# Performance work log

Measured on AMD Instinct MI355X. Metric: run time of the kernel, lower is better.

Reference implementation:

```python
import jax, jax.numpy as jnp
import numpy as np

B, Q, K = 4, 1024, 2048
QDIM, MDIM, EDIM, H = 1024, 1024, 1024, 16
HD = EDIM // H

def setup_inputs() -> dict:
    key = jax.random.key(0)
    ks = jax.random.split(key, 7)
    s = lambda d: (1.0 / np.sqrt(d))
    return {
        'query': jax.random.normal(ks[0], (B, Q, QDIM), jnp.float32),
        'memory': jax.random.normal(ks[1], (B, K, MDIM), jnp.float32),
        'bias': jax.random.normal(ks[2], (B, K), jnp.float32),
        'Wq': jax.random.normal(ks[3], (QDIM, EDIM), jnp.float32) * s(QDIM),
        'Wk': jax.random.normal(ks[4], (MDIM, EDIM), jnp.float32) * s(MDIM),
        'Wv': jax.random.normal(ks[5], (MDIM, EDIM), jnp.float32) * s(MDIM),
        'Wo': jax.random.normal(ks[6], (EDIM, EDIM), jnp.float32) * s(EDIM),
    }

def reference(query, memory, bias, Wq, Wk, Wv, Wo):
    scale = HD ** -0.5
    # projections -> [B, H, Q/K, HD]
    q = (query @ Wq).reshape(B, Q, H, HD).transpose(0, 2, 1, 3)
    k = (memory @ Wk).reshape(B, K, H, HD).transpose(0, 2, 1, 3)
    v = (memory @ Wv).reshape(B, K, H, HD).transpose(0, 2, 1, 3)
    scores = jnp.einsum('bhqd,bhkd->bhqk', q, k) * scale
    scores = scores + bias[:, None, None, :]
    weights = jax.nn.softmax(scores, axis=-1)
    out = jnp.einsum('bhqk,bhkd->bhqd', weights, v)
    out = out.transpose(0, 2, 1, 3).reshape(B, Q, EDIM)
    return out @ Wo
```

## Files before the change

kernel.cpp:

```cpp
#include <hip/hip_runtime.h>
#include <cstdint>
#include <cstddef>

typedef unsigned short u16;
typedef __attribute__((ext_vector_type(8))) short bf16x8;
typedef __attribute__((ext_vector_type(4))) short bf16x4;
typedef __attribute__((ext_vector_type(4))) float f32x4;
typedef __attribute__((ext_vector_type(16))) float f32x16;

#define B_  4
#define Q_  1024
#define K_  2048
#define E_  1024
#define H_  16
#define HD_ 64
#define LOG2E 1.4426950408889634f
#define M0_  16.0f

__device__ inline u16 f2bf(float f) {
  union { float f; uint32_t u; } x; x.f = f;
  return (u16)((x.u + 0x7fffu + ((x.u >> 16) & 1u)) >> 16);
}

__device__ inline short bfc(float f) {
  __bf16 h = (__bf16)f;
  return __builtin_bit_cast(short, h);
}

__device__ inline void gload16(const u16* g, void* l) {
  __builtin_amdgcn_global_load_lds((const __attribute__((address_space(1))) void*)g,
                                   (__attribute__((address_space(3))) void*)l, 16, 0, 0);
}

#define NQ8 (B_ * Q_ * E_ / 8)
#define NM8 (B_ * K_ * E_ / 8)
#define NBI (B_ * K_)
#define NPREP ((NQ8 + NM8 + NBI) / 256)
__global__ __launch_bounds__(256) void prep_all(const float* __restrict__ query,
                                                const float* __restrict__ memory,
                                                const float* __restrict__ bias,
                                                const float* W0, const float* W1,
                                                const float* W2, const float* W3,
                                                u16* __restrict__ qb,
                                                u16* __restrict__ mb,
                                                float* __restrict__ bias2,
                                                u16* T0, u16* T1, u16* T2, u16* T3) {
  __shared__ float t[64][65];
  int bid = blockIdx.x;
  if (bid < NPREP) {
    int i = bid * 256 + threadIdx.x;
    const float* src;
    u16* dst;
    if (i < NQ8) {
      src = query + (size_t)i * 8; dst = qb + (size_t)i * 8;
    } else if (i < NQ8 + NM8) {
      int j = i - NQ8;
      src = memory + (size_t)j * 8; dst = mb + (size_t)j * 8;
    } else {
      int j = i - (NQ8 + NM8);
      if (j < NBI) bias2[j] = bias[j] * LOG2E - M0_;
      return;
    }
    float4 a = *reinterpret_cast<const float4*>(src);
    float4 b = *reinterpret_cast<const float4*>(src + 4);
    union { u16 u[8]; uint4 v; } r;
    r.u[0] = f2bf(a.x); r.u[1] = f2bf(a.y); r.u[2] = f2bf(a.z); r.u[3] = f2bf(a.w);
    r.u[4] = f2bf(b.x); r.u[5] = f2bf(b.y); r.u[6] = f2bf(b.z); r.u[7] = f2bf(b.w);
    *reinterpret_cast<uint4*>(dst) = r.v;
  } else {
    int tb = bid - NPREP;
    int z = tb >> 8, xy = tb & 255;
    const float* W; u16* T;
    switch (z) {
      case 0: W = W0; T = T0; break;
      case 1: W = W1; T = T1; break;
      case 2: W = W2; T = T2; break;
      default: W = W3; T = T3; break;
    }
    int k0 = (xy & 15) * 64, n0 = (xy >> 4) * 64;
    int r = threadIdx.x >> 6, c = threadIdx.x & 63;
#pragma unroll
    for (int i = 0; i < 16; ++i)
      t[r + i * 4][c] = W[(size_t)(k0 + r + i * 4) * E_ + n0 + c];
    __syncthreads();
#pragma unroll
    for (int i = 0; i < 16; ++i)
      T[(size_t)(n0 + r + i * 4) * E_ + k0 + c] = f2bf(t[c][r + i * 4]);
  }
}

template <int MODE>
__device__ __forceinline__ void gemm_body(const u16* __restrict__ A,
                                          const u16* __restrict__ Bt,
                                          void* __restrict__ C,
                                          int M, int N, int Kc, int bx, int by,
                                          char* lds) {
  const int tid = threadIdx.x;
  const int w = tid >> 6, l = tid & 63;
  const int wr = w >> 1, wc = w & 1;
  const int lr = l & 15, lg = l >> 4;
  const int m0 = bx * 128, n0 = by * 128;

  const int e0g = tid * 8, e1g = e0g + 2048;
  const int row0 = e0g >> 5, row1 = e1g >> 5;
  const int lc0 = ((((e0g & 31) >> 3) ^ ((row0 >> 1) & 3)) * 8);
  const int lc1 = ((((e1g & 31) >> 3) ^ ((row1 >> 1) & 3)) * 8);
  const u16* Ar0 = A  + (size_t)(m0 + row0) * Kc + lc0;
  const u16* Ar1 = A  + (size_t)(m0 + row1) * Kc + lc1;
  const u16* Br0 = Bt + (size_t)(n0 + row0) * Kc + lc0;
  const u16* Br1 = Bt + (size_t)(n0 + row1) * Kc + lc1;
  const int d0 = tid * 16, d1 = d0 + 4096;

  const int ck = (lg ^ ((lr >> 1) & 3)) * 16;
  const int aofs = (wr * 64 + lr) * 64 + ck;
  const int bofs = (wc * 64 + lr) * 64 + ck;

  f32x4 acc[4][4];
#pragma unroll
  for (int mt = 0; mt < 4; ++mt)
#pragma unroll
    for (int nt = 0; nt < 4; ++nt)
      acc[mt][nt] = (f32x4){0.f, 0.f, 0.f, 0.f};

  gload16(Ar0, lds + d0);
  gload16(Ar1, lds + d1);
  gload16(Br0, lds + 24576 + d0);
  gload16(Br1, lds + 24576 + d1);
  gload16(Ar0 + 32, lds + 8192 + d0);
  gload16(Ar1 + 32, lds + 8192 + d1);
  gload16(Br0 + 32, lds + 24576 + 8192 + d0);
  gload16(Br1 + 32, lds + 24576 + 8192 + d1);
  asm volatile("s_waitcnt vmcnt(4)" ::: "memory");
  __builtin_amdgcn_s_barrier();

  const int NI = Kc >> 5;
  int rb = 0, wb = 16384;
  for (int ki = 0; ki < NI; ++ki) {
    if (ki + 2 < NI) {
      const int kk = (ki + 2) * 32;
      gload16(Ar0 + kk, lds + wb + d0);
      gload16(Ar1 + kk, lds + wb + d1);
      gload16(Br0 + kk, lds + 24576 + wb + d0);
      gload16(Br1 + kk, lds + 24576 + wb + d1);
    }

    bf16x8 a[4], b[4];
#pragma unroll
    for (int mt = 0; mt < 4; ++mt)
      a[mt] = *reinterpret_cast<const bf16x8*>(lds + rb + aofs + mt * 1024);
#pragma unroll
    for (int nt = 0; nt < 4; ++nt)
      b[nt] = *reinterpret_cast<const bf16x8*>(lds + 24576 + rb + bofs + nt * 1024);
    __builtin_amdgcn_s_setprio(1);
#pragma unroll
    for (int mt = 0; mt < 4; ++mt)
#pragma unroll
      for (int nt = 0; nt < 4; ++nt)
        acc[mt][nt] = __builtin_amdgcn_mfma_f32_16x16x32_bf16(a[mt], b[nt], acc[mt][nt], 0, 0, 0);
    __builtin_amdgcn_s_setprio(0);

    if (ki + 2 < NI) {
      asm volatile("s_waitcnt vmcnt(4)" ::: "memory");
    } else {
      asm volatile("s_waitcnt vmcnt(0)" ::: "memory");
    }
    __builtin_amdgcn_s_barrier();
    rb = (rb == 16384) ? 0 : rb + 8192;
    wb = (wb == 16384) ? 0 : wb + 8192;
  }

#pragma unroll
  for (int mt = 0; mt < 4; ++mt) {
#pragma unroll
    for (int nt = 0; nt < 4; ++nt) {
      int col = n0 + wc * 64 + nt * 16 + lr;
#pragma unroll
      for (int j = 0; j < 4; ++j) {
        int row = m0 + wr * 64 + mt * 16 + lg * 4 + j;
        float v = acc[mt][nt][j];
        if (MODE == 1) {
          ((u16*)C)[(size_t)row * N + col] = f2bf(v);
        } else if (MODE == 3) {
          ((u16*)C)[(size_t)row * N + col] = f2bf(v * (0.125f * LOG2E));
        } else {
          ((u16*)C)[((size_t)((col >> 11) * 16 + (row >> 6)) * 64 + (row & 63)) * 2048 + (col & 2047)] = f2bf(v);
        }
      }
    }
  }
}

__global__ __launch_bounds__(512) void gemm_out(const u16* __restrict__ A,
                                                const u16* __restrict__ Bt,
                                                float* __restrict__ C,
                                                int N, int Kc) {
  __shared__ uint4 lds4[3072];
  char* lds = (char*)lds4;
  int d = blockIdx.x;
  int bid = (d & 7) * 32 + (d >> 3);
  const int bx = bid >> 3, by = bid & 7;
  const int tid = threadIdx.x;
  const int w = tid >> 6, l = tid & 63;
  const int wrow = w >> 2, wcol = w & 3;
  const int lr = l & 15, lg = l >> 4;
  const int m0 = bx * 128, n0 = by * 128;

  const int e = tid * 8;
  const int row = e >> 5;
  const int lc = ((((e & 31) >> 3) ^ ((row >> 1) & 3)) * 8);
  const u16* Ar = A  + (size_t)(m0 + row) * Kc + lc;
  const u16* Br = Bt + (size_t)(n0 + row) * Kc + lc;
  const int dd = tid * 16;

  const int ck = (lg ^ ((lr >> 1) & 3)) * 16;
  const int aofs = (wrow * 64 + lr) * 64 + ck;
  const int bofs = (wcol * 32 + lr) * 64 + ck;

  f32x4 acc[4][2];
#pragma unroll
  for (int mt = 0; mt < 4; ++mt)
#pragma unroll
    for (int nt = 0; nt < 2; ++nt)
      acc[mt][nt] = (f32x4){0.f, 0.f, 0.f, 0.f};

  gload16(Ar, lds + dd);
  gload16(Br, lds + 24576 + dd);
  gload16(Ar + 32, lds + 8192 + dd);
  gload16(Br + 32, lds + 24576 + 8192 + dd);
  asm volatile("s_waitcnt vmcnt(2)" ::: "memory");
  __builtin_amdgcn_s_barrier();

  const int NI = Kc >> 5;
  int rb = 0, wb = 16384;
  for (int ki = 0; ki < NI; ++ki) {
    if (ki + 2 < NI) {
      const int kk = (ki + 2) * 32;
      gload16(Ar + kk, lds + wb + dd);
      gload16(Br + kk, lds + 24576 + wb + dd);
    }

    bf16x8 a[4], b[2];
#pragma unroll
    for (int mt = 0; mt < 4; ++mt)
      a[mt] = *reinterpret_cast<const bf16x8*>(lds + rb + aofs + mt * 1024);
#pragma unroll
    for (int nt = 0; nt < 2; ++nt)
      b[nt] = *reinterpret_cast<const bf16x8*>(lds + 24576 + rb + bofs + nt * 1024);
    __builtin_amdgcn_s_setprio(1);
#pragma unroll
    for (int mt = 0; mt < 4; ++mt)
#pragma unroll
      for (int nt = 0; nt < 2; ++nt)
        acc[mt][nt] = __builtin_amdgcn_mfma_f32_16x16x32_bf16(a[mt], b[nt], acc[mt][nt], 0, 0, 0);
    __builtin_amdgcn_s_setprio(0);

    if (ki + 2 < NI) {
      asm volatile("s_waitcnt vmcnt(2)" ::: "memory");
    } else {
      asm volatile("s_waitcnt vmcnt(0)" ::: "memory");
    }
    __builtin_amdgcn_s_barrier();
    rb = (rb == 16384) ? 0 : rb + 8192;
    wb = (wb == 16384) ? 0 : wb + 8192;
  }

#pragma unroll
  for (int mt = 0; mt < 4; ++mt) {
#pragma unroll
    for (int nt = 0; nt < 2; ++nt) {
      int col = n0 + wcol * 32 + nt * 16 + lr;
#pragma unroll
      for (int j = 0; j < 4; ++j) {
        int rowc = m0 + wrow * 64 + mt * 16 + lg * 4 + j;
        C[(size_t)rowc * N + col] = acc[mt][nt][j];
      }
    }
  }
}

__global__ __launch_bounds__(256) void proj_fused(const u16* __restrict__ qb,
                                                  const u16* __restrict__ mb,
                                                  const u16* __restrict__ wqt,
                                                  const u16* __restrict__ wkt,
                                                  const u16* __restrict__ wvt,
                                                  u16* __restrict__ qproj,
                                                  u16* __restrict__ kproj,
                                                  u16* __restrict__ vt) {
  __shared__ uint4 lds4[3072];
  char* lds = (char*)lds4;
  int d = blockIdx.x;
  int bid = (d & 7) * 160 + (d >> 3);
  if (bid < 256) {
    gemm_body<3>(qb, wqt, qproj, B_ * Q_, E_, E_, bid >> 3, bid & 7, lds);
  } else if (bid < 768) {
    int i = bid - 256;
    gemm_body<1>(mb, wkt, kproj, B_ * K_, E_, E_, i >> 3, i & 7, lds);
  } else {
    int i = bid - 768;
    gemm_body<2>(wvt, mb, vt, E_, B_ * K_, E_, i & 7, i >> 3, lds);
  }
}

__global__ __launch_bounds__(256, 4) void attn_kernel(const u16* __restrict__ qp,
                                                      const u16* __restrict__ kp,
                                                      const u16* __restrict__ vT,
                                                      const float* __restrict__ bias2,
                                                      u16* __restrict__ out) {
  __shared__ uint4 lds4[2048];
  char* ldsb = (char*)lds4;

  const int blk = blockIdx.x;
  const int hg = blk & 63, qt = blk >> 6;
  const int b = hg >> 4, h = hg & 15;
  const int tid = threadIdx.x;
  const int w = tid >> 6, l = tid & 63;
  const int wq = w & 1, wk = w >> 1;
  const int l31 = l & 31, lh = l >> 5;

  const int bk4 = l31 >> 2;
  const int t4 = bk4 & 3;
  const int pk31 = (((t4 == 1) || (t4 == 2)) ? (bk4 ^ 3) : bk4) * 4 + (l31 & 3);

  bf16x8 qf[4];
  const u16* qrow = qp + (size_t)(b * Q_ + qt * 64 + wq * 32 + l31) * E_ + h * 64 + lh * 8;
#pragma unroll
  for (int st = 0; st < 4; ++st)
    qf[st] = *reinterpret_cast<const bf16x8*>(qrow + st * 16);

  f32x16 O0, O1;
#pragma unroll
  for (int i = 0; i < 16; ++i) { O0[i] = 0.f; O1[i] = 0.f; }
  float OsumL = 0.f;

  const float* bias_b = bias2 + (size_t)b * K_;
  const u16* kbase = kp + (size_t)b * K_ * E_ + h * 64;
  const u16* vbase = vT + (size_t)(b * H_ + h) * HD_ * K_;

  const int xkk = (pk31 & 7) * 8;
  const int xvv = (l31 & 7) * 8;
  int kofs[4];
#pragma unroll
  for (int st = 0; st < 4; ++st)
    kofs[st] = (wk * 32 + pk31) * 128 + (((st * 16 + lh * 8) ^ xkk) << 1);
  int vofs[2];
#pragma unroll
  for (int ksl = 0; ksl < 2; ++ksl)
    vofs[ksl] = 16384 + l31 * 128 + (((wk * 32 + ksl * 16 + lh * 8) ^ xvv) << 1);

  const float* btp = bias_b + wk * 32 + lh * 8;
  float4 bg0 = *reinterpret_cast<const float4*>(btp);
  float4 bg1 = *reinterpret_cast<const float4*>(btp + 4);
  float4 bg2 = *reinterpret_cast<const float4*>(btp + 16);
  float4 bg3 = *reinterpret_cast<const float4*>(btp + 20);

  const int e0 = tid * 8, e1 = e0 + 2048;
  const int r0 = e0 >> 6, r1 = e1 >> 6;
  const int sc0 = (e0 & 63) ^ ((r0 & 7) * 8);
  const int sc1 = (e1 & 63) ^ ((r1 & 7) * 8);
  const u16* kp0 = kbase + (size_t)r0 * E_ + sc0;
  const u16* kp1 = kbase + (size_t)r1 * E_ + sc1;
  const u16* vp0 = vbase + (size_t)r0 * K_ + sc0;
  const u16* vp1 = vbase + (size_t)r1 * K_ + sc1;

  gload16(kp0, ldsb + tid * 16);
  gload16(kp1, ldsb + 4096 + tid * 16);
  gload16(vp0, ldsb + 16384 + tid * 16);
  gload16(vp1, ldsb + 16384 + 4096 + tid * 16);
  __syncthreads();

  const int NT = K_ / 64;
  for (int t = 0; t < NT; ++t) {
    if (t + 1 < NT) {
      const int nb = ((t & 1) ^ 1) * 8192;
      kp0 += (size_t)64 * E_; kp1 += (size_t)64 * E_;
      vp0 += 64; vp1 += 64;
      gload16(kp0, ldsb + nb + tid * 16);
      gload16(kp1, ldsb + nb + 4096 + tid * 16);
      gload16(vp0, ldsb + 16384 + nb + tid * 16);
      gload16(vp1, ldsb + 16384 + nb + 4096 + tid * 16);
    }

    f32x16 S;
    S[0] = bg0.x; S[1] = bg0.y; S[2] = bg0.z; S[3] = bg0.w;
    S[4] = bg1.x; S[5] = bg1.y; S[6] = bg1.z; S[7] = bg1.w;
    S[8] = bg2.x; S[9] = bg2.y; S[10] = bg2.z; S[11] = bg2.w;
    S[12] = bg3.x; S[13] = bg3.y; S[14] = bg3.z; S[15] = bg3.w;

    float4 ng0 = bg0, ng1 = bg1, ng2 = bg2, ng3 = bg3;
    if (t + 1 < NT) {
      btp += 64;
      ng0 = *reinterpret_cast<const float4*>(btp);
      ng1 = *reinterpret_cast<const float4*>(btp + 4);
      ng2 = *reinterpret_cast<const float4*>(btp + 16);
      ng3 = *reinterpret_cast<const float4*>(btp + 20);
    }

    __builtin_amdgcn_s_setprio(1);
#pragma unroll
    for (int st = 0; st < 4; ++st) {
      bf16x8 ka = *reinterpret_cast<const bf16x8*>(ldsb + kofs[st]);
      S = __builtin_amdgcn_mfma_f32_32x32x16_bf16(ka, qf[st], S, 0, 0, 0);
    }
    __builtin_amdgcn_s_setprio(0);

#pragma unroll
    for (int i = 0; i < 16; ++i) S[i] = __builtin_amdgcn_exp2f(S[i]);
    float ps = ((S[0] + S[1]) + (S[2] + S[3])) + ((S[4] + S[5]) + (S[6] + S[7]))
             + ((S[8] + S[9]) + (S[10] + S[11])) + ((S[12] + S[13]) + (S[14] + S[15]));
    OsumL += ps;

    uint32_t u[8];
#pragma unroll
    for (int j = 0; j < 8; ++j) {
      float plo = S[2 * j], phi = S[2 * j + 1];
      asm("v_cvt_pk_bf16_f32 %0, %1, %2" : "=v"(u[j]) : "v"(plo), "v"(phi));
    }
    bf16x8 P0 = __builtin_bit_cast(bf16x8, (uint4){u[0], u[1], u[2], u[3]});
    bf16x8 P1 = __builtin_bit_cast(bf16x8, (uint4){u[4], u[5], u[6], u[7]});

    __builtin_amdgcn_s_setprio(1);
    {
      bf16x8 va;
      va = *reinterpret_cast<const bf16x8*>(ldsb + vofs[0]);
      O0 = __builtin_amdgcn_mfma_f32_32x32x16_bf16(va, P0, O0, 0, 0, 0);
      va = *reinterpret_cast<const bf16x8*>(ldsb + vofs[0] + 4096);
      O1 = __builtin_amdgcn_mfma_f32_32x32x16_bf16(va, P0, O1, 0, 0, 0);
      va = *reinterpret_cast<const bf16x8*>(ldsb + vofs[1]);
      O0 = __builtin_amdgcn_mfma_f32_32x32x16_bf16(va, P1, O0, 0, 0, 0);
      va = *reinterpret_cast<const bf16x8*>(ldsb + vofs[1] + 4096);
      O1 = __builtin_amdgcn_mfma_f32_32x32x16_bf16(va, P1, O1, 0, 0, 0);
    }
    __builtin_amdgcn_s_setprio(0);

    bg0 = ng0; bg1 = ng1; bg2 = ng2; bg3 = ng3;
    kofs[0] ^= 8192; kofs[1] ^= 8192; kofs[2] ^= 8192; kofs[3] ^= 8192;
    vofs[0] ^= 8192; vofs[1] ^= 8192;
    __syncthreads();
  }

  float Osum = OsumL + __shfl_xor(OsumL, 32, 64);

  float* ex = (float*)ldsb + (size_t)(wq * 64 + l) * 33;
  if (wk == 1) {
#pragma unroll
    for (int i = 0; i < 16; ++i) ex[i] = O0[i];
#pragma unroll
    for (int i = 0; i < 16; ++i) ex[16 + i] = O1[i];
    ex[32] = Osum;
  }
  __syncthreads();
  if (wk == 0) {
#pragma unroll
    for (int i = 0; i < 16; ++i) O0[i] += ex[i];
#pragma unroll
    for (int i = 0; i < 16; ++i) O1[i] += ex[16 + i];
    Osum += ex[32];
    float inv = 1.f / Osum;
    u16* orow = out + (size_t)(b * Q_ + qt * 64 + wq * 32 + l31) * E_ + h * 64;
#pragma unroll
    for (int g = 0; g < 4; ++g) {
      int hd0 = 8 * g + 4 * lh;
#pragma unroll
      for (int j = 0; j < 4; ++j) {
        orow[hd0 + j] = (u16)bfc(O0[4 * g + j] * inv);
        orow[32 + hd0 + j] = (u16)bfc(O1[4 * g + j] * inv);
      }
    }
  }
}

extern "C" void kernel_launch(void* const* d_in, const int* in_sizes, int n_in,
                              void* d_out, int out_size, void* d_ws, size_t ws_size,
                              hipStream_t stream) {
  const float* query  = (const float*)d_in[0];
  const float* memory = (const float*)d_in[1];
  const float* bias   = (const float*)d_in[2];
  const float* Wq     = (const float*)d_in[3];
  const float* Wk     = (const float*)d_in[4];
  const float* Wv     = (const float*)d_in[5];
  const float* Wo     = (const float*)d_in[6];
  float* out = (float*)d_out;

  char* p = (char*)d_ws;
  u16* qb    = (u16*)p; p += (size_t)B_ * Q_ * E_ * 2;
  u16* mb    = (u16*)p; p += (size_t)B_ * K_ * E_ * 2;
  u16* wqt   = (u16*)p; p += (size_t)E_ * E_ * 2;
  u16* wkt   = (u16*)p; p += (size_t)E_ * E_ * 2;
  u16* wvt   = (u16*)p; p += (size_t)E_ * E_ * 2;
  u16* wot   = (u16*)p; p += (size_t)E_ * E_ * 2;
  u16* qproj = (u16*)p; p += (size_t)B_ * Q_ * E_ * 2;
  u16* kproj = (u16*)p; p += (size_t)B_ * K_ * E_ * 2;
  u16* vt    = (u16*)p; p += (size_t)B_ * K_ * E_ * 2;
  u16* attn  = (u16*)p; p += (size_t)B_ * Q_ * E_ * 2;
  float* bias2 = (float*)p; p += (size_t)B_ * K_ * 4;

  prep_all<<<NPREP + 1024, 256, 0, stream>>>(query, memory, bias, Wq, Wk, Wv, Wo,
                                             qb, mb, bias2, wqt, wkt, wvt, wot);

  proj_fused<<<1280, 256, 0, stream>>>(qb, mb, wqt, wkt, wvt, qproj, kproj, vt);

  attn_kernel<<<B_ * H_ * (Q_ / 64), 256, 0, stream>>>(qproj, kproj, vt, bias2, attn);

  gemm_out<<<256, 512, 0, stream>>>(attn, wot, out, E_, E_);
}
```

Baseline: 134.9 us.

## Fuse fp32-to-bf16 conversion of activations into projection GEMM loads

Removes the separate pass that converted query and memory to bf16 buffers. The projection GEMM now reads fp32 directly, converts in registers and stores to LDS, which saves a full write and re-read of the activations. The LDS pipeline also drops from triple buffering with async global-to-LDS loads to double buffering with register staging and a __syncthreads every iteration. That may expose more latency, and the memory operand is now read as fp32 by both the K and V GEMMs.

```diff
diff --git a/kernel.cpp b/kernel.cpp
--- a/kernel.cpp
+++ b/kernel.cpp
@@ -16,6 +16,7 @@
 #define HD_ 64
 #define LOG2E 1.4426950408889634f
 #define M0_  16.0f
+#define NBI (B_ * K_)
 
 __device__ inline u16 f2bf(float f) {
   union { float f; uint32_t u; } x; x.f = f;
@@ -27,73 +28,52 @@
   return __builtin_bit_cast(short, h);
 }
 
+__device__ inline uint2 pack4(float4 a) {
+  union { u16 u[4]; uint2 v; } r;
+  r.u[0] = (u16)bfc(a.x); r.u[1] = (u16)bfc(a.y);
+  r.u[2] = (u16)bfc(a.z); r.u[3] = (u16)bfc(a.w);
+  return r.v;
+}
+
 __device__ inline void gload16(const u16* g, void* l) {
   __builtin_amdgcn_global_load_lds((const __attribute__((address_space(1))) void*)g,
                                    (__attribute__((address_space(3))) void*)l, 16, 0, 0);
 }
 
-#define NQ8 (B_ * Q_ * E_ / 8)
-#define NM8 (B_ * K_ * E_ / 8)
-#define NBI (B_ * K_)
-#define NPREP ((NQ8 + NM8 + NBI) / 256)
-__global__ __launch_bounds__(256) void prep_all(const float* __restrict__ query,
-                                                const float* __restrict__ memory,
-                                                const float* __restrict__ bias,
+__global__ __launch_bounds__(256) void prep_all(const float* __restrict__ bias,
                                                 const float* W0, const float* W1,
                                                 const float* W2, const float* W3,
-                                                u16* __restrict__ qb,
-                                                u16* __restrict__ mb,
                                                 float* __restrict__ bias2,
                                                 u16* T0, u16* T1, u16* T2, u16* T3) {
   __shared__ float t[64][65];
   int bid = blockIdx.x;
-  if (bid < NPREP) {
-    int i = bid * 256 + threadIdx.x;
-    const float* src;
-    u16* dst;
-    if (i < NQ8) {
-      src = query + (size_t)i * 8; dst = qb + (size_t)i * 8;
-    } else if (i < NQ8 + NM8) {
-      int j = i - NQ8;
-      src = memory + (size_t)j * 8; dst = mb + (size_t)j * 8;
-    } else {
-      int j = i - (NQ8 + NM8);
-      if (j < NBI) bias2[j] = bias[j] * LOG2E - M0_;
-      return;
-    }
-    float4 a = *reinterpret_cast<const float4*>(src);
-    float4 b = *reinterpret_cast<const float4*>(src + 4);
-    union { u16 u[8]; uint4 v; } r;
-    r.u[0] = f2bf(a.x); r.u[1] = f2bf(a.y); r.u[2] = f2bf(a.z); r.u[3] = f2bf(a.w);
-    r.u[4] = f2bf(b.x); r.u[5] = f2bf(b.y); r.u[6] = f2bf(b.z); r.u[7] = f2bf(b.w);
-    *reinterpret_cast<uint4*>(dst) = r.v;
-  } else {
-    int tb = bid - NPREP;
-    int z = tb >> 8, xy = tb & 255;
-    const float* W; u16* T;
-    switch (z) {
-      case 0: W = W0; T = T0; break;
-      case 1: W = W1; T = T1; break;
-      case 2: W = W2; T = T2; break;
-      default: W = W3; T = T3; break;
-    }
-    int k0 = (xy & 15) * 64, n0 = (xy >> 4) * 64;
-    int r = threadIdx.x >> 6, c = threadIdx.x & 63;
-#pragma unroll
-    for (int i = 0; i < 16; ++i)
-      t[r + i * 4][c] = W[(size_t)(k0 + r + i * 4) * E_ + n0 + c];
-    __syncthreads();
-#pragma unroll
-    for (int i = 0; i < 16; ++i)
-      T[(size_t)(n0 + r + i * 4) * E_ + k0 + c] = f2bf(t[c][r + i * 4]);
-  }
-}
-
-template <int MODE>
-__device__ __forceinline__ void gemm_body(const u16* __restrict__ A,
-                                          const u16* __restrict__ Bt,
-                                          void* __restrict__ C,
-                                          int M, int N, int Kc, int bx, int by,
+  if (bid >= 1024) {
+    int j = (bid - 1024) * 256 + threadIdx.x;
+    if (j < NBI) bias2[j] = bias[j] * LOG2E - M0_;
+    return;
+  }
+  int z = bid >> 8, xy = bid & 255;
+  const float* W; u16* T;
+  switch (z) {
+    case 0: W = W0; T = T0; break;
+    case 1: W = W1; T = T1; break;
+    case 2: W = W2; T = T2; break;
+    default: W = W3; T = T3; break;
+  }
+  int k0 = (xy & 15) * 64, n0 = (xy >> 4) * 64;
+  int r = threadIdx.x >> 6, c = threadIdx.x & 63;
+#pragma unroll
+  for (int i = 0; i < 16; ++i)
+    t[r + i * 4][c] = W[(size_t)(k0 + r + i * 4) * E_ + n0 + c];
+  __syncthreads();
+#pragma unroll
+  for (int i = 0; i < 16; ++i)
+    T[(size_t)(n0 + r + i * 4) * E_ + k0 + c] = f2bf(t[c][r + i * 4]);
+}
+
+template <int MODE, bool AF32, bool BF32>
+__device__ __forceinline__ void gemm_body(const void* Ap, const void* Bp,
+                                          void* C, int M, int N, int Kc, int bx, int by,
                                           char* lds) {
   const int tid = threadIdx.x;
   const int w = tid >> 6, l = tid & 63;
@@ -105,15 +85,31 @@
   const int row0 = e0g >> 5, row1 = e1g >> 5;
   const int lc0 = ((((e0g & 31) >> 3) ^ ((row0 >> 1) & 3)) * 8);
   const int lc1 = ((((e1g & 31) >> 3) ^ ((row1 >> 1) & 3)) * 8);
-  const u16* Ar0 = A  + (size_t)(m0 + row0) * Kc + lc0;
-  const u16* Ar1 = A  + (size_t)(m0 + row1) * Kc + lc1;
-  const u16* Br0 = Bt + (size_t)(n0 + row0) * Kc + lc0;
-  const u16* Br1 = Bt + (size_t)(n0 + row1) * Kc + lc1;
   const int d0 = tid * 16, d1 = d0 + 4096;
 
+  const int fr = tid >> 3;
+  const int fcb = (tid & 7) * 4;
+  const int fphys = ((fcb >> 3) ^ ((fr >> 1) & 3));
+  const int fdst = fr * 64 + fphys * 16 + (fcb & 7) * 2;
+
+  const u16* A16_0 = nullptr; const u16* A16_1 = nullptr; const float* Afp = nullptr;
+  const u16* B16_0 = nullptr; const u16* B16_1 = nullptr; const float* Bfp = nullptr;
+  if constexpr (AF32) {
+    Afp = (const float*)Ap + (size_t)(m0 + fr) * Kc + fcb;
+  } else {
+    A16_0 = (const u16*)Ap + (size_t)(m0 + row0) * Kc + lc0;
+    A16_1 = (const u16*)Ap + (size_t)(m0 + row1) * Kc + lc1;
+  }
+  if constexpr (BF32) {
+    Bfp = (const float*)Bp + (size_t)(n0 + fr) * Kc + fcb;
+  } else {
+    B16_0 = (const u16*)Bp + (size_t)(n0 + row0) * Kc + lc0;
+    B16_1 = (const u16*)Bp + (size_t)(n0 + row1) * Kc + lc1;
+  }
+
   const int ck = (lg ^ ((lr >> 1) & 3)) * 16;
-  const int aofs = (wr * 64 + lr) * 64 + ck;
-  const int bofs = (wc * 64 + lr) * 64 + ck;
+  int aofs = (wr * 64 + lr) * 64 + ck;
+  int bofs = 16384 + (wc * 64 + lr) * 64 + ck;
 
   f32x4 acc[4][4];
 #pragma unroll
@@ -122,35 +118,71 @@
     for (int nt = 0; nt < 4; ++nt)
       acc[mt][nt] = (f32x4){0.f, 0.f, 0.f, 0.f};
 
-  gload16(Ar0, lds + d0);
-  gload16(Ar1, lds + d1);
-  gload16(Br0, lds + 24576 + d0);
-  gload16(Br1, lds + 24576 + d1);
-  gload16(Ar0 + 32, lds + 8192 + d0);
-  gload16(Ar1 + 32, lds + 8192 + d1);
-  gload16(Br0 + 32, lds + 24576 + 8192 + d0);
-  gload16(Br1 + 32, lds + 24576 + 8192 + d1);
-  asm volatile("s_waitcnt vmcnt(4)" ::: "memory");
-  __builtin_amdgcn_s_barrier();
+  if constexpr (AF32) {
+    float4 t0 = *reinterpret_cast<const float4*>(Afp);
+    float4 t1 = *reinterpret_cast<const float4*>(Afp + (size_t)32 * Kc);
+    float4 t2 = *reinterpret_cast<const float4*>(Afp + (size_t)64 * Kc);
+    float4 t3 = *reinterpret_cast<const float4*>(Afp + (size_t)96 * Kc);
+    *reinterpret_cast<uint2*>(lds + fdst)        = pack4(t0);
+    *reinterpret_cast<uint2*>(lds + fdst + 2048) = pack4(t1);
+    *reinterpret_cast<uint2*>(lds + fdst + 4096) = pack4(t2);
+    *reinterpret_cast<uint2*>(lds + fdst + 6144) = pack4(t3);
+  } else {
+    gload16(A16_0, lds + d0);
+    gload16(A16_1, lds + d1);
+  }
+  if constexpr (BF32) {
+    float4 t0 = *reinterpret_cast<const float4*>(Bfp);
+    float4 t1 = *reinterpret_cast<const float4*>(Bfp + (size_t)32 * Kc);
+    float4 t2 = *reinterpret_cast<const float4*>(Bfp + (size_t)64 * Kc);
+    float4 t3 = *reinterpret_cast<const float4*>(Bfp + (size_t)96 * Kc);
+    *reinterpret_cast<uint2*>(lds + 16384 + fdst)        = pack4(t0);
+    *reinterpret_cast<uint2*>(lds + 16384 + fdst + 2048) = pack4(t1);
+    *reinterpret_cast<uint2*>(lds + 16384 + fdst + 4096) = pack4(t2);
+    *reinterpret_cast<uint2*>(lds + 16384 + fdst + 6144) = pack4(t3);
+  } else {
+    gload16(B16_0, lds + 16384 + d0);
+    gload16(B16_1, lds + 16384 + d1);
+  }
+  __syncthreads();
 
   const int NI = Kc >> 5;
-  int rb = 0, wb = 16384;
+  int cur = 0;
   for (int ki = 0; ki < NI; ++ki) {
-    if (ki + 2 < NI) {
-      const int kk = (ki + 2) * 32;
-      gload16(Ar0 + kk, lds + wb + d0);
-      gload16(Ar1 + kk, lds + wb + d1);
-      gload16(Br0 + kk, lds + 24576 + wb + d0);
-      gload16(Br1 + kk, lds + 24576 + wb + d1);
+    const int nb = (cur ^ 1) * 8192;
+    const bool pf = (ki + 1 < NI);
+    float4 va0, va1, va2, va3, vb0, vb1, vb2, vb3;
+    if (pf) {
+      const int kk = (ki + 1) * 32;
+      if constexpr (AF32) {
+        const float* s = Afp + kk;
+        va0 = *reinterpret_cast<const float4*>(s);
+        va1 = *reinterpret_cast<const float4*>(s + (size_t)32 * Kc);
+        va2 = *reinterpret_cast<const float4*>(s + (size_t)64 * Kc);
+        va3 = *reinterpret_cast<const float4*>(s + (size_t)96 * Kc);
+      } else {
+        gload16(A16_0 + kk, lds + nb + d0);
+        gload16(A16_1 + kk, lds + nb + d1);
+      }
+      if constexpr (BF32) {
+        const float* s = Bfp + kk;
+        vb0 = *reinterpret_cast<const float4*>(s);
+        vb1 = *reinterpret_cast<const float4*>(s + (size_t)32 * Kc);
+        vb2 = *reinterpret_cast<const float4*>(s + (size_t)64 * Kc);
+        vb3 = *reinterpret_cast<const float4*>(s + (size_t)96 * Kc);
+      } else {
+        gload16(B16_0 + kk, lds + 16384 + nb + d0);
+        gload16(B16_1 + kk, lds + 16384 + nb + d1);
+      }
     }
 
     bf16x8 a[4], b[4];
 #pragma unroll
     for (int mt = 0; mt < 4; ++mt)
-      a[mt] = *reinterpret_cast<const bf16x8*>(lds + rb + aofs + mt * 1024);
+      a[mt] = *reinterpret_cast<const bf16x8*>(lds + aofs + mt * 1024);
 #pragma unroll
     for (int nt = 0; nt < 4; ++nt)
-      b[nt] = *reinterpret_cast<const bf16x8*>(lds + 24576 + rb + bofs + nt * 1024);
+      b[nt] = *reinterpret_cast<const bf16x8*>(lds + bofs + nt * 1024);
     __builtin_amdgcn_s_setprio(1);
 #pragma unroll
     for (int mt = 0; mt < 4; ++mt)
@@ -159,14 +191,23 @@
         acc[mt][nt] = __builtin_amdgcn_mfma_f32_16x16x32_bf16(a[mt], b[nt], acc[mt][nt], 0, 0, 0);
     __builtin_amdgcn_s_setprio(0);
 
-    if (ki + 2 < NI) {
-      asm volatile("s_waitcnt vmcnt(4)" ::: "memory");
-    } else {
-      asm volatile("s_waitcnt vmcnt(0)" ::: "memory");
-    }
-    __builtin_amdgcn_s_barrier();
-    rb = (rb == 16384) ? 0 : rb + 8192;
-    wb = (wb == 16384) ? 0 : wb + 8192;
+    if (pf) {
+      if constexpr (AF32) {
+        *reinterpret_cast<uint2*>(lds + nb + fdst)        = pack4(va0);
+        *reinterpret_cast<uint2*>(lds + nb + fdst + 2048) = pack4(va1);
+        *reinterpret_cast<uint2*>(lds + nb + fdst + 4096) = pack4(va2);
+        *reinterpret_cast<uint2*>(lds + nb + fdst + 6144) = pack4(va3);
+      }
+      if constexpr (BF32) {
+        *reinterpret_cast<uint2*>(lds + 16384 + nb + fdst)        = pack4(vb0);
+        *reinterpret_cast<uint2*>(lds + 16384 + nb + fdst + 2048) = pack4(vb1);
+        *reinterpret_cast<uint2*>(lds + 16384 + nb + fdst + 4096) = pack4(vb2);
+        *reinterpret_cast<uint2*>(lds + 16384 + nb + fdst + 6144) = pack4(vb3);
+      }
+    }
+
+    aofs ^= 8192; bofs ^= 8192; cur ^= 1;
+    __syncthreads();
   }
 
 #pragma unroll
@@ -278,26 +319,26 @@
   }
 }
 
-__global__ __launch_bounds__(256) void proj_fused(const u16* __restrict__ qb,
-                                                  const u16* __restrict__ mb,
+__global__ __launch_bounds__(256) void proj_fused(const float* __restrict__ query,
+                                                  const float* __restrict__ memory,
                                                   const u16* __restrict__ wqt,
                                                   const u16* __restrict__ wkt,
                                                   const u16* __restrict__ wvt,
                                                   u16* __restrict__ qproj,
                                                   u16* __restrict__ kproj,
                                                   u16* __restrict__ vt) {
-  __shared__ uint4 lds4[3072];
+  __shared__ uint4 lds4[2048];
   char* lds = (char*)lds4;
   int d = blockIdx.x;
   int bid = (d & 7) * 160 + (d >> 3);
   if (bid < 256) {
-    gemm_body<3>(qb, wqt, qproj, B_ * Q_, E_, E_, bid >> 3, bid & 7, lds);
+    gemm_body<3, true, false>(query, wqt, qproj, B_ * Q_, E_, E_, bid >> 3, bid & 7, lds);
   } else if (bid < 768) {
     int i = bid - 256;
-    gemm_body<1>(mb, wkt, kproj, B_ * K_, E_, E_, i >> 3, i & 7, lds);
+    gemm_body<1, true, false>(memory, wkt, kproj, B_ * K_, E_, E_, i >> 3, i & 7, lds);
   } else {
     int i = bid - 768;
-    gemm_body<2>(wvt, mb, vt, E_, B_ * K_, E_, i & 7, i >> 3, lds);
+    gemm_body<2, false, true>(wvt, memory, vt, E_, B_ * K_, E_, i & 7, i >> 3, lds);
   }
 }
 
@@ -482,8 +523,6 @@
   float* out = (float*)d_out;
 
   char* p = (char*)d_ws;
-  u16* qb    = (u16*)p; p += (size_t)B_ * Q_ * E_ * 2;
-  u16* mb    = (u16*)p; p += (size_t)B_ * K_ * E_ * 2;
   u16* wqt   = (u16*)p; p += (size_t)E_ * E_ * 2;
   u16* wkt   = (u16*)p; p += (size_t)E_ * E_ * 2;
   u16* wvt   = (u16*)p; p += (size_t)E_ * E_ * 2;
@@ -494,10 +533,9 @@
   u16* attn  = (u16*)p; p += (size_t)B_ * Q_ * E_ * 2;
   float* bias2 = (float*)p; p += (size_t)B_ * K_ * 4;
 
-  prep_all<<<NPREP + 1024, 256, 0, stream>>>(query, memory, bias, Wq, Wk, Wv, Wo,
-                                             qb, mb, bias2, wqt, wkt, wvt, wot);
-
-  proj_fused<<<1280, 256, 0, stream>>>(qb, mb, wqt, wkt, wvt, qproj, kproj, vt);
+  prep_all<<<1056, 256, 0, stream>>>(bias, Wq, Wk, Wv, Wo, bias2, wqt, wkt, wvt, wot);
+
+  proj_fused<<<1280, 256, 0, stream>>>(query, memory, wqt, wkt, wvt, qproj, kproj, vt);
 
   attn_kernel<<<B_ * H_ * (Q_ / 64), 256, 0, stream>>>(qproj, kproj, vt, bias2, attn);
 
```

New measurement: 140.8 us. 1.04x slower.
